# Kernel optimization log

Hardware: AMD Instinct MI355X
Metric: run time of the kernel (lower is better)

The kernel has to match this reference:

```python
import jax, jax.numpy as jnp
import numpy as np

N_AGENTS = 8
N_HEADS = 4
HYP = 128   # hypernet_embed
EMB = 32    # mixing_embed_dim


def _hypernet(entities, entity_mask, fc1_w, fc1_b, attn_w, out_w, out_b, fc2_w, fc2_b):
    # entities: [B, ne, ed]; entity_mask: [B, ne] (1 = masked/inactive)
    B, ne, _ = entities.shape
    hd = HYP // N_HEADS
    x1 = jax.nn.relu(entities @ fc1_w + fc1_b)                      # [B, ne, HYP]
    am = entity_mask[:, :N_AGENTS].astype(x1.dtype)                 # [B, na]
    em = entity_mask.astype(x1.dtype)                               # [B, ne]
    # attn_mask[b,i,j] = 1 - (1-am[i])*(1-em[j]): mask if agent i OR entity j inactive
    pre_mask = 1.0 - (1.0 - am)[:, :, None] * (1.0 - em)[:, None, :]  # [B, na, ne]
    # EntityAttentionLayer: agents are the queries, all entities are keys/values
    qkv = x1 @ attn_w                                               # [B, ne, 3*HYP] (no bias)
    q, k, v = jnp.split(qkv, 3, axis=-1)
    q = q[:, :N_AGENTS].reshape(B, N_AGENTS, N_HEADS, hd)
    k = k.reshape(B, ne, N_HEADS, hd)
    v = v.reshape(B, ne, N_HEADS, hd)
    scale = jnp.asarray(np.sqrt(hd), x1.dtype)
    logits = jnp.einsum('bqhd,bkhd->bhqk', q, k) / scale            # [B, H, na, ne]
    m = pre_mask[:, None, :, :]
    # masked softmax; fully-masked rows (torch: -inf -> NaN -> 0) become 0 via *(1-m)
    w = jax.nn.softmax(jnp.where(m > 0, -1e30, logits), axis=-1) * (1.0 - m)
    attn = jnp.einsum('bhqk,bkhd->bqhd', w, v).reshape(B, N_AGENTS, HYP)
    attn = attn @ out_w + out_b                                     # [B, na, HYP]
    keep = (1.0 - am)[:, :, None]                                   # zero masked agents (post_mask)
    attn = attn * keep
    x3 = (attn @ fc2_w + fc2_b) * keep                              # [B, na, EMB]
    return x3


def reference(agent_qs, entities, entity_mask, fc1_w, fc1_b, attn_w, out_w, out_b, fc2_w, fc2_b):
    bs, T, ne, ed = entities.shape
    B = bs * T
    ents = entities.reshape(B, ne, ed)
    emask = entity_mask.reshape(B, ne)
    qs = agent_qs.reshape(B, N_AGENTS)
    # 4 hypernets: 0=hyper_w_1 (matrix), 1=hyper_w_final (vector), 2=hyper_b_1 (vector), 3=V (scalar)
    outs = [_hypernet(ents, emask, fc1_w[i], fc1_b[i], attn_w[i], out_w[i],
                      out_b[i], fc2_w[i], fc2_b[i]) for i in range(4)]
    w1 = jax.nn.softmax(outs[0], axis=-1)                           # [B, na, EMB]
    b1 = outs[2].mean(axis=1)                                       # [B, EMB]
    hidden = jax.nn.elu(jnp.einsum('ba,bae->be', qs, w1) + b1)      # [B, EMB]
    w_final = jax.nn.softmax(outs[1].mean(axis=1), axis=-1)         # [B, EMB]
    v = outs[3].mean(axis=(1, 2))                                   # [B]
    y = jnp.sum(hidden * w_final, axis=-1) + v                      # [B]
    return y.reshape(bs, T, 1)


def setup_inputs() -> dict:
    key = jax.random.key(0)
    ks = jax.random.split(key, 10)
    bs, T, ne, ed = 128, 64, 16, 64
    s = 0.05
    return {
        'agent_qs': jax.random.normal(ks[0], (bs, T, N_AGENTS), jnp.float32),
        'entities': jax.random.normal(ks[1], (bs, T, ne, ed), jnp.float32),
        'entity_mask': jax.random.randint(ks[2], (bs, T, ne), 0, 2, jnp.int32),
        'fc1_w': jax.random.normal(ks[3], (4, ed, HYP), jnp.float32) * s,
        'fc1_b': jax.random.normal(ks[4], (4, HYP), jnp.float32) * s,
        'attn_w': jax.random.normal(ks[5], (4, HYP, 3 * HYP), jnp.float32) * s,
        'out_w': jax.random.normal(ks[6], (4, HYP, HYP), jnp.float32) * s,
        'out_b': jax.random.normal(ks[7], (4, HYP), jnp.float32) * s,
        'fc2_w': jax.random.normal(ks[8], (4, HYP, EMB), jnp.float32) * s,
        'fc2_b': jax.random.normal(ks[9], (4, EMB), jnp.float32) * s,
    }
```

## Files before the change

kernel.cpp:

```cpp
#include <hip/hip_runtime.h>
#include <math.h>

#define NAG 8
#define NE  16
#define ED  64
#define HYPD 128
#define QKVW 384
#define SB 4

#define X1S 132
#define KS  132
#define QS  132

#define WARENA 11520
#define LDS_BYTES (4 * WARENA)

typedef __attribute__((ext_vector_type(8))) short bf16x8;
typedef __attribute__((ext_vector_type(4))) short bf16x4;
typedef __attribute__((ext_vector_type(4))) float f32x4;

__device__ __forceinline__ short f2bf(float f) {
    union { float f; unsigned u; } c; c.f = f;
    unsigned r = (c.u + 0x7FFFu + ((c.u >> 16) & 1u)) >> 16;
    return (short)r;
}
__device__ __forceinline__ float bf2f(short s) {
    union { unsigned u; float f; } c; c.u = ((unsigned)(unsigned short)s) << 16; return c.f;
}
__device__ __forceinline__ bf16x8 ld_frag(const short* p) {
    bf16x4 lo = *(const bf16x4*)p;
    bf16x4 hi = *(const bf16x4*)(p + 16);
    return __builtin_shufflevector(lo, hi, 0, 1, 2, 3, 4, 5, 6, 7);
}

__global__ void pack_weights(const float* __restrict__ fc1_w,
                             const float* __restrict__ attn_w,
                             const float* __restrict__ out_w,
                             const float* __restrict__ fc2_w,
                             short* __restrict__ ws) {
    int gid = blockIdx.x * 256 + threadIdx.x;
    if (gid >= 608 * 64) return;
    int slot = gid >> 6, l = gid & 63;
    const float* src; int N, nt, kt;
    if (slot < 64) {
        int h = slot >> 4, f = slot & 15;
        nt = f >> 1; kt = f & 1; N = HYPD; src = fc1_w + h * ED * HYPD;
    } else if (slot < 448) {
        int s2 = slot - 64; int h = s2 / 96, f = s2 % 96;
        nt = f >> 2; kt = f & 3; N = QKVW; src = attn_w + h * HYPD * QKVW;
    } else if (slot < 576) {
        int s2 = slot - 448; int h = s2 >> 5, f = s2 & 31;
        nt = f >> 2; kt = f & 3; N = HYPD; src = out_w + h * HYPD * HYPD;
    } else {
        int s2 = slot - 576; int h = s2 >> 3, f = s2 & 7;
        nt = f >> 2; kt = f & 3; N = 32; src = fc2_w + h * HYPD * 32;
    }
    int rg = l >> 4, lc = l & 15;
    bf16x8 fr;
    #pragma unroll
    for (int j = 0; j < 8; ++j) {
        int k = kt * 32 + 4 * rg + (j & 3) + 16 * (j >> 2);
        fr[j] = f2bf(src[k * N + nt * 16 + lc]);
    }
    ((bf16x8*)ws)[slot * 64 + l] = fr;
}

__global__ __launch_bounds__(256, 2) void flexq_mfma(
    const float* __restrict__ agent_qs,
    const float* __restrict__ entities,
    const int*   __restrict__ entity_mask,
    const float* __restrict__ fc1_b,
    const float* __restrict__ out_b,
    const float* __restrict__ fc2_b,
    const short* __restrict__ wfrag,
    float* __restrict__ out, int B)
{
    __shared__ __align__(16) char smem[LDS_BYTES];
    const int tid = threadIdx.x;
    const int l = tid & 63, w = tid >> 6;
    const int rg = l >> 4, lc = l & 15;
    const int ss = blockIdx.x * SB + w;
    const bf16x8* WF = (const bf16x8*)wfrag;

    char* ws0 = smem + w * WARENA;
    short* x1    = (short*)(ws0);
    float* slog  = (float*)(ws0);
    short* attn  = (short*)(ws0 + 2112);
    short* k     = (short*)(ws0 + 4224);
    short* attn2 = (short*)(ws0 + 4224);
    short* q     = (short*)(ws0 + 8448);
    short* out0  = (short*)(ws0 + 10560);
    float* means = (float*)(ws0 + 11072);
    float* em    = (float*)(ws0 + 11456);

    if (l < 16)
        em[l] = (entity_mask[(size_t)ss * NE + l] != 0) ? 1.0f : 0.0f;

    bf16x8 aent[2];
    #pragma unroll
    for (int kt = 0; kt < 2; ++kt) {
        const float* ap = entities + ((size_t)ss * NE + lc) * ED + kt * 32 + rg * 4;
        float4 lo = *(const float4*)ap;
        float4 hi = *(const float4*)(ap + 16);
        bf16x8 af;
        af[0]=f2bf(lo.x); af[1]=f2bf(lo.y); af[2]=f2bf(lo.z); af[3]=f2bf(lo.w);
        af[4]=f2bf(hi.x); af[5]=f2bf(hi.y); af[6]=f2bf(hi.z); af[7]=f2bf(hi.w);
        aent[kt] = af;
    }

    for (int i = 0; i < 4; ++i) {
        {
            f32x4 acc[8];
            #pragma unroll
            for (int n = 0; n < 8; ++n) acc[n] = (f32x4){0.f,0.f,0.f,0.f};
            #pragma unroll
            for (int kt = 0; kt < 2; ++kt)
                #pragma unroll
                for (int n = 0; n < 8; ++n) {
                    bf16x8 bn = WF[(i*16 + n*2 + kt)*64 + l];
                    acc[n] = __builtin_amdgcn_mfma_f32_16x16x32_bf16(aent[kt], bn, acc[n], 0,0,0);
                }
            #pragma unroll
            for (int n = 0; n < 8; ++n) {
                float bias = fc1_b[i*HYPD + n*16 + lc];
                #pragma unroll
                for (int r = 0; r < 4; ++r)
                    x1[(4*rg + r)*X1S + n*16 + lc] = f2bf(fmaxf(acc[n][r] + bias, 0.f));
            }
        }

        f32x4 accv[8];
        {
            f32x4 acc[8];
            #pragma unroll
            for (int n = 0; n < 8; ++n) acc[n] = (f32x4){0.f,0.f,0.f,0.f};
            #pragma unroll
            for (int kt = 0; kt < 4; ++kt) {
                bf16x8 a = ld_frag(x1 + lc*X1S + kt*32 + rg*4);
                #pragma unroll
                for (int n = 0; n < 8; ++n) {
                    bf16x8 bn = WF[(64 + i*96 + n*4 + kt)*64 + l];
                    acc[n] = __builtin_amdgcn_mfma_f32_16x16x32_bf16(a, bn, acc[n], 0,0,0);
                }
            }
            if (rg < 2) {
                #pragma unroll
                for (int n = 0; n < 8; ++n)
                    #pragma unroll
                    for (int r = 0; r < 4; ++r)
                        q[(4*rg + r)*QS + n*16 + lc] = f2bf(acc[n][r]);
            }
        }
        {
            f32x4 acc[8];
            #pragma unroll
            for (int n = 0; n < 8; ++n) acc[n] = (f32x4){0.f,0.f,0.f,0.f};
            #pragma unroll
            for (int kt = 0; kt < 4; ++kt) {
                bf16x8 a = ld_frag(x1 + lc*X1S + kt*32 + rg*4);
                #pragma unroll
                for (int n = 0; n < 8; ++n) {
                    bf16x8 bn = WF[(64 + i*96 + (8 + n)*4 + kt)*64 + l];
                    acc[n] = __builtin_amdgcn_mfma_f32_16x16x32_bf16(a, bn, acc[n], 0,0,0);
                }
            }
            #pragma unroll
            for (int n = 0; n < 8; ++n)
                #pragma unroll
                for (int r = 0; r < 4; ++r)
                    k[(4*rg + r)*KS + n*16 + lc] = f2bf(acc[n][r]);
        }
        {
            #pragma unroll
            for (int n = 0; n < 8; ++n) accv[n] = (f32x4){0.f,0.f,0.f,0.f};
            #pragma unroll
            for (int kt = 0; kt < 4; ++kt) {
                bf16x8 a = ld_frag(x1 + lc*X1S + kt*32 + rg*4);
                #pragma unroll
                for (int n = 0; n < 8; ++n) {
                    bf16x8 bn = WF[(64 + i*96 + (16 + n)*4 + kt)*64 + l];
                    accv[n] = __builtin_amdgcn_mfma_f32_16x16x32_bf16(a, bn, accv[n], 0,0,0);
                }
            }
        }

        {
            #pragma unroll
            for (int h = 0; h < 4; ++h) {
                bf16x8 a  = ld_frag(q + (lc & 7)*QS + h*32 + rg*4);
                bf16x8 bb = ld_frag(k + lc*KS       + h*32 + rg*4);
                f32x4 acc = (f32x4){0.f,0.f,0.f,0.f};
                acc = __builtin_amdgcn_mfma_f32_16x16x32_bf16(a, bb, acc, 0,0,0);
                if (rg < 2) {
                    #pragma unroll
                    for (int r = 0; r < 4; ++r)
                        slog[(h*NAG + 4*rg + r)*16 + lc] = acc[r] * 0.17677669529663687f;
                }
            }
        }

        if (l < 32) {
            int qi = l & 7;
            float am = em[qi];
            float* rowp = slog + l*16;
            float mx = -3.0e38f; bool any = false;
            #pragma unroll
            for (int kk = 0; kk < NE; ++kk)
                if (em[kk] == 0.f) { any = true; mx = fmaxf(mx, rowp[kk]); }
            if (am != 0.f || !any) {
                #pragma unroll
                for (int kk = 0; kk < NE; ++kk) rowp[kk] = 0.f;
            } else {
                float eb[NE]; float sum = 0.f;
                #pragma unroll
                for (int kk = 0; kk < NE; ++kk) {
                    float e = (em[kk] == 0.f) ? __expf(rowp[kk] - mx) : 0.f;
                    eb[kk] = e; sum += e;
                }
                float inv = 1.f / sum;
                #pragma unroll
                for (int kk = 0; kk < NE; ++kk) rowp[kk] = eb[kk] * inv;
            }
        }

        {
            #pragma unroll
            for (int c = 0; c < 8; ++c) {
                int h = c >> 1;
                f32x4 pw = *(const f32x4*)(slog + (h*NAG + (lc & 7))*16 + 4*rg);
                bf16x8 a;
                a[0]=f2bf(pw[0]); a[1]=f2bf(pw[1]); a[2]=f2bf(pw[2]); a[3]=f2bf(pw[3]);
                a[4]=0; a[5]=0; a[6]=0; a[7]=0;
                bf16x8 bb;
                bb[0]=f2bf(accv[c][0]); bb[1]=f2bf(accv[c][1]);
                bb[2]=f2bf(accv[c][2]); bb[3]=f2bf(accv[c][3]);
                bb[4]=0; bb[5]=0; bb[6]=0; bb[7]=0;
                f32x4 po = (f32x4){0.f,0.f,0.f,0.f};
                po = __builtin_amdgcn_mfma_f32_16x16x32_bf16(a, bb, po, 0,0,0);
                if (rg < 2) {
                    #pragma unroll
                    for (int r = 0; r < 4; ++r)
                        attn[(4*rg + r)*X1S + c*16 + lc] = f2bf(po[r]);
                }
            }
        }

        {
            f32x4 acc[8];
            #pragma unroll
            for (int n = 0; n < 8; ++n) acc[n] = (f32x4){0.f,0.f,0.f,0.f};
            #pragma unroll
            for (int kt = 0; kt < 4; ++kt) {
                bf16x8 a = ld_frag(attn + lc*X1S + kt*32 + rg*4);
                #pragma unroll
                for (int n = 0; n < 8; ++n) {
                    bf16x8 bn = WF[(448 + i*32 + n*4 + kt)*64 + l];
                    acc[n] = __builtin_amdgcn_mfma_f32_16x16x32_bf16(a, bn, acc[n], 0,0,0);
                }
            }
            if (rg < 2) {
                #pragma unroll
                for (int n = 0; n < 8; ++n) {
                    float bias = out_b[i*HYPD + n*16 + lc];
                    #pragma unroll
                    for (int r = 0; r < 4; ++r) {
                        int row = 4*rg + r;
                        float keep = 1.f - em[row];
                        attn2[row*X1S + n*16 + lc] = f2bf((acc[n][r] + bias) * keep);
                    }
                }
            }
        }

        {
            f32x4 acc[2];
            acc[0] = (f32x4){0.f,0.f,0.f,0.f};
            acc[1] = (f32x4){0.f,0.f,0.f,0.f};
            #pragma unroll
            for (int kt = 0; kt < 4; ++kt) {
                bf16x8 a = ld_frag(attn2 + lc*X1S + kt*32 + rg*4);
                #pragma unroll
                for (int n = 0; n < 2; ++n) {
                    bf16x8 bn = WF[(576 + i*8 + n*4 + kt)*64 + l];
                    acc[n] = __builtin_amdgcn_mfma_f32_16x16x32_bf16(a, bn, acc[n], 0,0,0);
                }
            }
            #pragma unroll
            for (int n = 0; n < 2; ++n) {
                float bias = fc2_b[i*32 + n*16 + lc];
                float vals[4];
                #pragma unroll
                for (int r = 0; r < 4; ++r) {
                    int row = 4*rg + r;
                    float keep = (row < 8) ? (1.f - em[row]) : 0.f;
                    vals[r] = (acc[n][r] + bias) * keep;
                }
                if (i == 0) {
                    if (rg < 2)
                        #pragma unroll
                        for (int r = 0; r < 4; ++r)
                            out0[(4*rg + r)*32 + n*16 + lc] = f2bf(vals[r]);
                } else {
                    float ps = vals[0] + vals[1] + vals[2] + vals[3];
                    ps += __shfl_xor(ps, 16);
                    if (rg == 0)
                        means[(i-1)*32 + n*16 + lc] = ps;
                }
            }
        }
    }

    if (l < 32) {
        int c = l;
        float s1 = means[0*32 + c] * 0.125f;
        float b1 = means[1*32 + c] * 0.125f;
        float vsum = means[2*32 + c];

        float hid = 0.f;
        #pragma unroll
        for (int a = 0; a < NAG; ++a) {
            float x = bf2f(out0[a*32 + c]);
            float mx = x;
            #pragma unroll
            for (int m = 16; m >= 1; m >>= 1) mx = fmaxf(mx, __shfl_xor(mx, m, 32));
            float e = __expf(x - mx);
            float sum = e;
            #pragma unroll
            for (int m = 16; m >= 1; m >>= 1) sum += __shfl_xor(sum, m, 32);
            float qsv = agent_qs[(size_t)ss*NAG + a];
            hid += qsv * (e / sum);
        }
        hid += b1;
        hid = (hid > 0.f) ? hid : expm1f(hid);

        float mx = s1;
        #pragma unroll
        for (int m = 16; m >= 1; m >>= 1) mx = fmaxf(mx, __shfl_xor(mx, m, 32));
        float e = __expf(s1 - mx);
        float ssm = e;
        #pragma unroll
        for (int m = 16; m >= 1; m >>= 1) ssm += __shfl_xor(ssm, m, 32);
        float wf = e / ssm;

        float red = hid * wf + vsum * (1.f / 256.f);
        #pragma unroll
        for (int m = 16; m >= 1; m >>= 1) red += __shfl_xor(red, m, 32);
        if (c == 0) out[ss] = red;
    }
}

#define QKVP 388
#define NTHR 384
__device__ __forceinline__ float4 f4load(const float* p) { return *reinterpret_cast<const float4*>(p); }
__device__ __forceinline__ void f4store(float* p, const float4& v) { *reinterpret_cast<float4*>(p) = v; }
__device__ __forceinline__ void f4fma(float4& a, float s, const float4& w) {
    a.x += s * w.x; a.y += s * w.y; a.z += s * w.z; a.w += s * w.w;
}

__global__ __launch_bounds__(NTHR) void flexq_fp32(
    const float* __restrict__ agent_qs, const float* __restrict__ entities,
    const int* __restrict__ entity_mask, const float* __restrict__ fc1_w,
    const float* __restrict__ fc1_b, const float* __restrict__ attn_w,
    const float* __restrict__ out_w, const float* __restrict__ out_b,
    const float* __restrict__ fc2_w, const float* __restrict__ fc2_b,
    float* __restrict__ out)
{
    const int b = blockIdx.x, tid = threadIdx.x;
    __shared__ float s_ent[NE][ED];
    __shared__ float s_x1t[HYPD][NE];
    __shared__ float s_qkv[NE][QKVP];
    __shared__ float s_w[4][NAG][NE];
    __shared__ float s_attn[NAG][HYPD];
    __shared__ float s_attnout[NAG][HYPD];
    __shared__ float s_outs[4][NAG][32];
    __shared__ float s_mask[NE];
    __shared__ float s_qs[NAG];

    const float* ent = entities + (size_t)b * NE * ED;
    for (int o = tid; o < NE * ED; o += NTHR) s_ent[o >> 6][o & 63] = ent[o];
    if (tid < NE) s_mask[tid] = (entity_mask[(size_t)b * NE + tid] != 0) ? 1.0f : 0.0f;
    if (tid < NAG) s_qs[tid] = agent_qs[(size_t)b * NAG + tid];
    __syncthreads();

    for (int i = 0; i < 4; ++i) {
        {
            const float* W1 = fc1_w + i * ED * HYPD;
            const float* B1 = fc1_b + i * HYPD;
            for (int o4 = tid; o4 < 512; o4 += NTHR) {
                int e = o4 >> 5, j = (o4 & 31) * 4;
                float4 acc = f4load(B1 + j);
                for (int d = 0; d < ED; ++d) { float x = s_ent[e][d]; f4fma(acc, x, f4load(W1 + d * HYPD + j)); }
                s_x1t[j+0][e] = fmaxf(acc.x, 0.f); s_x1t[j+1][e] = fmaxf(acc.y, 0.f);
                s_x1t[j+2][e] = fmaxf(acc.z, 0.f); s_x1t[j+3][e] = fmaxf(acc.w, 0.f);
            }
        }
        __syncthreads();
        {
            const float* W2 = attn_w + i * HYPD * QKVW;
            int j = (tid % 96) * 4, e0 = (tid / 96) * 4;
            float4 a0 = {0,0,0,0}, a1 = {0,0,0,0}, a2 = {0,0,0,0}, a3 = {0,0,0,0};
            for (int d = 0; d < HYPD; ++d) {
                float4 wv = f4load(W2 + d * QKVW + j);
                float4 x = f4load(&s_x1t[d][e0]);
                f4fma(a0, x.x, wv); f4fma(a1, x.y, wv); f4fma(a2, x.z, wv); f4fma(a3, x.w, wv);
            }
            f4store(&s_qkv[e0+0][j], a0); f4store(&s_qkv[e0+1][j], a1);
            f4store(&s_qkv[e0+2][j], a2); f4store(&s_qkv[e0+3][j], a3);
        }
        __syncthreads();
        {
            const float inv_scale = 0.17677669529663687f;
            for (int o = tid; o < 512; o += NTHR) {
                int h = o >> 7, qi = (o >> 4) & 7, kk = o & 15;
                const float* qp = &s_qkv[qi][h * 32];
                const float* kp = &s_qkv[kk][HYPD + h * 32];
                float s = 0.f;
                #pragma unroll
                for (int d4 = 0; d4 < 8; ++d4) {
                    float4 qv = f4load(qp + 4 * d4), kv2 = f4load(kp + 4 * d4);
                    s += qv.x*kv2.x + qv.y*kv2.y + qv.z*kv2.z + qv.w*kv2.w;
                }
                s_w[h][qi][kk] = s * inv_scale;
            }
        }
        __syncthreads();
        if (tid < 32) {
            int h = tid >> 3, qi = tid & 7;
            float am = s_mask[qi];
            float mx = -3.0e38f; bool any = false;
            #pragma unroll
            for (int kk = 0; kk < NE; ++kk)
                if (s_mask[kk] == 0.f) { any = true; mx = fmaxf(mx, s_w[h][qi][kk]); }
            if (am != 0.f || !any) {
                #pragma unroll
                for (int kk = 0; kk < NE; ++kk) s_w[h][qi][kk] = 0.f;
            } else {
                float eb[NE]; float sum = 0.f;
                #pragma unroll
                for (int kk = 0; kk < NE; ++kk) {
                    float e = (s_mask[kk] == 0.f) ? __expf(s_w[h][qi][kk] - mx) : 0.f;
                    eb[kk] = e; sum += e;
                }
                float inv = 1.f / sum;
                #pragma unroll
                for (int kk = 0; kk < NE; ++kk) s_w[h][qi][kk] = eb[kk] * inv;
            }
        }
        __syncthreads();
        if (tid < 256) {
            int qi = tid >> 5, j = (tid & 31) * 4, h = j >> 5, d0 = j & 31;
            float4 acc = {0,0,0,0};
            #pragma unroll
            for (int kk = 0; kk < NE; ++kk) f4fma(acc, s_w[h][qi][kk], f4load(&s_qkv[kk][2*HYPD + h*32 + d0]));
            f4store(&s_attn[qi][j], acc);
        }
        __syncthreads();
        if (tid < 256) {
            const float* W3 = out_w + i * HYPD * HYPD;
            const float* B3 = out_b + i * HYPD;
            int qi = tid >> 5, j = (tid & 31) * 4;
            float4 acc = f4load(B3 + j);
            for (int d = 0; d < HYPD; ++d) f4fma(acc, s_attn[qi][d], f4load(W3 + d * HYPD + j));
            float keep = 1.f - s_mask[qi];
            acc.x *= keep; acc.y *= keep; acc.z *= keep; acc.w *= keep;
            f4store(&s_attnout[qi][j], acc);
        }
        __syncthreads();
        if (tid < 64) {
            const float* W4 = fc2_w + i * HYPD * 32;
            const float* B4 = fc2_b + i * 32;
            int qi = tid >> 3, c = (tid & 7) * 4;
            float4 acc = f4load(B4 + c);
            for (int d = 0; d < HYPD; ++d) f4fma(acc, s_attnout[qi][d], f4load(W4 + d * 32 + c));
            float keep = 1.f - s_mask[qi];
            acc.x *= keep; acc.y *= keep; acc.z *= keep; acc.w *= keep;
            f4store(&s_outs[i][qi][c], acc);
        }
        __syncthreads();
    }

    if (tid < 32) {
        const int c = tid;
        float b1 = 0.f, s1 = 0.f, vs = 0.f;
        #pragma unroll
        for (int qi = 0; qi < NAG; ++qi) {
            b1 += s_outs[2][qi][c]; s1 += s_outs[1][qi][c]; vs += s_outs[3][qi][c];
        }
        b1 *= 0.125f; s1 *= 0.125f;
        float hid = 0.f;
        #pragma unroll
        for (int a = 0; a < NAG; ++a) {
            float x = s_outs[0][a][c];
            float mx = x;
            #pragma unroll
            for (int m = 16; m >= 1; m >>= 1) mx = fmaxf(mx, __shfl_xor(mx, m, 32));
            float e = __expf(x - mx);
            float sm = e;
            #pragma unroll
            for (int m = 16; m >= 1; m >>= 1) sm += __shfl_xor(sm, m, 32);
            hid += s_qs[a] * (e / sm);
        }
        hid += b1;
        hid = (hid > 0.f) ? hid : expm1f(hid);
        float mx = s1;
        #pragma unroll
        for (int m = 16; m >= 1; m >>= 1) mx = fmaxf(mx, __shfl_xor(mx, m, 32));
        float e = __expf(s1 - mx);
        float ssum = e;
        #pragma unroll
        for (int m = 16; m >= 1; m >>= 1) ssum += __shfl_xor(ssum, m, 32);
        float wf = e / ssum;
        float red = hid * wf + vs * (1.f / 256.f);
        #pragma unroll
        for (int m = 16; m >= 1; m >>= 1) red += __shfl_xor(red, m, 32);
        if (tid == 0) out[b] = red;
    }
}

extern "C" void kernel_launch(void* const* d_in, const int* in_sizes, int n_in,
                              void* d_out, int out_size, void* d_ws, size_t ws_size,
                              hipStream_t stream) {
    const float* agent_qs    = (const float*)d_in[0];
    const float* entities    = (const float*)d_in[1];
    const int*   entity_mask = (const int*)  d_in[2];
    const float* fc1_w       = (const float*)d_in[3];
    const float* fc1_b       = (const float*)d_in[4];
    const float* attn_w      = (const float*)d_in[5];
    const float* out_w       = (const float*)d_in[6];
    const float* out_b       = (const float*)d_in[7];
    const float* fc2_w       = (const float*)d_in[8];
    const float* fc2_b       = (const float*)d_in[9];
    float* out = (float*)d_out;

    const int B = in_sizes[0] / NAG;

    if (ws_size >= (size_t)(608 * 1024) && (B % SB) == 0) {
        pack_weights<<<152, 256, 0, stream>>>(fc1_w, attn_w, out_w, fc2_w, (short*)d_ws);
        flexq_mfma<<<B / SB, 256, 0, stream>>>(agent_qs, entities, entity_mask,
                                               fc1_b, out_b, fc2_b,
                                               (const short*)d_ws, out, B);
    } else {
        flexq_fp32<<<B, NTHR, 0, stream>>>(agent_qs, entities, entity_mask,
                                           fc1_w, fc1_b, attn_w, out_w, out_b,
                                           fc2_w, fc2_b, out);
    }
}
```

Baseline: 192.8 us.

## Shrink per-wave LDS arena and compute masked softmax in registers via shuffles

Cuts the per-wave LDS arena from 11520 to 8192 bytes by aliasing buffers, storing the mask as shorts, padding rows to 130 and storing probabilities as bf16. The V projection now runs before K so K can overwrite x1. The masked softmax moves from a serial 32-lane loop into a cross-lane shuffle reduction on the MFMA output. Fragment loads for attention rows use lc&7 so buffers only hold 8 rows. The aim is fewer LDS bytes and a shorter serial softmax, at the risk of bank conflicts from the odd padding and more registers held live.

```diff
diff --git a/kernel.cpp b/kernel.cpp
--- a/kernel.cpp
+++ b/kernel.cpp
@@ -8,11 +8,17 @@
 #define QKVW 384
 #define SB 4
 
-#define X1S 132
-#define KS  132
-#define QS  132
-
-#define WARENA 11520
+#define X1S 130
+#define KS  130
+#define QS  130
+
+#define OFF_A     0
+#define OFF_B     4160
+#define OFF_SLOGB 6240
+#define OFF_OUT0  7264
+#define OFF_MEANS 7776
+#define OFF_EM    8160
+#define WARENA 8192
 #define LDS_BYTES (4 * WARENA)
 
 typedef __attribute__((ext_vector_type(8))) short bf16x8;
@@ -83,18 +89,18 @@
     const bf16x8* WF = (const bf16x8*)wfrag;
 
     char* ws0 = smem + w * WARENA;
-    short* x1    = (short*)(ws0);
-    float* slog  = (float*)(ws0);
-    short* attn  = (short*)(ws0 + 2112);
-    short* k     = (short*)(ws0 + 4224);
-    short* attn2 = (short*)(ws0 + 4224);
-    short* q     = (short*)(ws0 + 8448);
-    short* out0  = (short*)(ws0 + 10560);
-    float* means = (float*)(ws0 + 11072);
-    float* em    = (float*)(ws0 + 11456);
+    short* x1    = (short*)(ws0 + OFF_A);
+    short* k     = (short*)(ws0 + OFF_A);
+    short* attn2 = (short*)(ws0 + OFF_A);
+    short* q     = (short*)(ws0 + OFF_B);
+    short* attn  = (short*)(ws0 + OFF_B);
+    short* slogb = (short*)(ws0 + OFF_SLOGB);
+    short* out0  = (short*)(ws0 + OFF_OUT0);
+    float* means = (float*)(ws0 + OFF_MEANS);
+    short* em    = (short*)(ws0 + OFF_EM);
 
     if (l < 16)
-        em[l] = (entity_mask[(size_t)ss * NE + l] != 0) ? 1.0f : 0.0f;
+        em[l] = (entity_mask[(size_t)ss * NE + l] != 0) ? 1 : 0;
 
     bf16x8 aent[2];
     #pragma unroll
@@ -152,6 +158,19 @@
             }
         }
         {
+            #pragma unroll
+            for (int n = 0; n < 8; ++n) accv[n] = (f32x4){0.f,0.f,0.f,0.f};
+            #pragma unroll
+            for (int kt = 0; kt < 4; ++kt) {
+                bf16x8 a = ld_frag(x1 + lc*X1S + kt*32 + rg*4);
+                #pragma unroll
+                for (int n = 0; n < 8; ++n) {
+                    bf16x8 bn = WF[(64 + i*96 + (16 + n)*4 + kt)*64 + l];
+                    accv[n] = __builtin_amdgcn_mfma_f32_16x16x32_bf16(a, bn, accv[n], 0,0,0);
+                }
+            }
+        }
+        {
             f32x4 acc[8];
             #pragma unroll
             for (int n = 0; n < 8; ++n) acc[n] = (f32x4){0.f,0.f,0.f,0.f};
@@ -170,56 +189,33 @@
                 for (int r = 0; r < 4; ++r)
                     k[(4*rg + r)*KS + n*16 + lc] = f2bf(acc[n][r]);
         }
-        {
-            #pragma unroll
-            for (int n = 0; n < 8; ++n) accv[n] = (f32x4){0.f,0.f,0.f,0.f};
-            #pragma unroll
-            for (int kt = 0; kt < 4; ++kt) {
-                bf16x8 a = ld_frag(x1 + lc*X1S + kt*32 + rg*4);
-                #pragma unroll
-                for (int n = 0; n < 8; ++n) {
-                    bf16x8 bn = WF[(64 + i*96 + (16 + n)*4 + kt)*64 + l];
-                    accv[n] = __builtin_amdgcn_mfma_f32_16x16x32_bf16(a, bn, accv[n], 0,0,0);
-                }
-            }
-        }
-
-        {
+
+        {
+            short myem = em[lc];
+            bool evalid = (myem == 0);
             #pragma unroll
             for (int h = 0; h < 4; ++h) {
                 bf16x8 a  = ld_frag(q + (lc & 7)*QS + h*32 + rg*4);
                 bf16x8 bb = ld_frag(k + lc*KS       + h*32 + rg*4);
                 f32x4 acc = (f32x4){0.f,0.f,0.f,0.f};
                 acc = __builtin_amdgcn_mfma_f32_16x16x32_bf16(a, bb, acc, 0,0,0);
-                if (rg < 2) {
+                #pragma unroll
+                for (int r = 0; r < 4; ++r) {
+                    float L = acc[r] * 0.17677669529663687f;
+                    float mv = evalid ? L : -3.0e38f;
                     #pragma unroll
-                    for (int r = 0; r < 4; ++r)
-                        slog[(h*NAG + 4*rg + r)*16 + lc] = acc[r] * 0.17677669529663687f;
-                }
-            }
-        }
-
-        if (l < 32) {
-            int qi = l & 7;
-            float am = em[qi];
-            float* rowp = slog + l*16;
-            float mx = -3.0e38f; bool any = false;
-            #pragma unroll
-            for (int kk = 0; kk < NE; ++kk)
-                if (em[kk] == 0.f) { any = true; mx = fmaxf(mx, rowp[kk]); }
-            if (am != 0.f || !any) {
-                #pragma unroll
-                for (int kk = 0; kk < NE; ++kk) rowp[kk] = 0.f;
-            } else {
-                float eb[NE]; float sum = 0.f;
-                #pragma unroll
-                for (int kk = 0; kk < NE; ++kk) {
-                    float e = (em[kk] == 0.f) ? __expf(rowp[kk] - mx) : 0.f;
-                    eb[kk] = e; sum += e;
-                }
-                float inv = 1.f / sum;
-                #pragma unroll
-                for (int kk = 0; kk < NE; ++kk) rowp[kk] = eb[kk] * inv;
+                    for (int m = 1; m <= 8; m <<= 1) mv = fmaxf(mv, __shfl_xor(mv, m));
+                    float ex = evalid ? __expf(L - mv) : 0.f;
+                    float sm = ex;
+                    #pragma unroll
+                    for (int m = 1; m <= 8; m <<= 1) sm += __shfl_xor(sm, m);
+                    bool any = (mv > -1.0e37f);
+                    int row = 4*rg + r;
+                    bool am_nz = (em[row & 15] != 0);
+                    float P = (am_nz || !any) ? 0.f : ex / sm;
+                    if (rg < 2)
+                        slogb[(h*NAG + row)*16 + lc] = f2bf(P);
+                }
             }
         }
 
@@ -227,9 +223,9 @@
             #pragma unroll
             for (int c = 0; c < 8; ++c) {
                 int h = c >> 1;
-                f32x4 pw = *(const f32x4*)(slog + (h*NAG + (lc & 7))*16 + 4*rg);
+                bf16x4 plo = *(const bf16x4*)(slogb + (h*NAG + (lc & 7))*16 + 4*rg);
                 bf16x8 a;
-                a[0]=f2bf(pw[0]); a[1]=f2bf(pw[1]); a[2]=f2bf(pw[2]); a[3]=f2bf(pw[3]);
+                a[0]=plo[0]; a[1]=plo[1]; a[2]=plo[2]; a[3]=plo[3];
                 a[4]=0; a[5]=0; a[6]=0; a[7]=0;
                 bf16x8 bb;
                 bb[0]=f2bf(accv[c][0]); bb[1]=f2bf(accv[c][1]);
@@ -251,7 +247,7 @@
             for (int n = 0; n < 8; ++n) acc[n] = (f32x4){0.f,0.f,0.f,0.f};
             #pragma unroll
             for (int kt = 0; kt < 4; ++kt) {
-                bf16x8 a = ld_frag(attn + lc*X1S + kt*32 + rg*4);
+                bf16x8 a = ld_frag(attn + (lc & 7)*X1S + kt*32 + rg*4);
                 #pragma unroll
                 for (int n = 0; n < 8; ++n) {
                     bf16x8 bn = WF[(448 + i*32 + n*4 + kt)*64 + l];
@@ -265,7 +261,7 @@
                     #pragma unroll
                     for (int r = 0; r < 4; ++r) {
                         int row = 4*rg + r;
-                        float keep = 1.f - em[row];
+                        float keep = em[row] ? 0.f : 1.f;
                         attn2[row*X1S + n*16 + lc] = f2bf((acc[n][r] + bias) * keep);
                     }
                 }
@@ -278,7 +274,7 @@
             acc[1] = (f32x4){0.f,0.f,0.f,0.f};
             #pragma unroll
             for (int kt = 0; kt < 4; ++kt) {
-                bf16x8 a = ld_frag(attn2 + lc*X1S + kt*32 + rg*4);
+                bf16x8 a = ld_frag(attn2 + (lc & 7)*X1S + kt*32 + rg*4);
                 #pragma unroll
                 for (int n = 0; n < 2; ++n) {
                     bf16x8 bn = WF[(576 + i*8 + n*4 + kt)*64 + l];
@@ -292,7 +288,7 @@
                 #pragma unroll
                 for (int r = 0; r < 4; ++r) {
                     int row = 4*rg + r;
-                    float keep = (row < 8) ? (1.f - em[row]) : 0.f;
+                    float keep = (row < 8) ? (em[row] ? 0.f : 1.f) : 0.f;
                     vals[r] = (acc[n][r] + bias) * keep;
                 }
                 if (i == 0) {
```

New measurement: 354.8 us. +84.0%, slower.
